# Performance work log

Measured on AMD Instinct MI355X. Metric: run time of the kernel, lower is better.

## Reference

```python
import jax, jax.numpy as jnp
import numpy as np

DIM = 192
HEADS = 8
HEAD_DIM = DIM // HEADS
SCALE = HEAD_DIM ** (-0.5)
H = W = 64
EPS = 1e-12  # F.normalize default eps


def setup_inputs() -> dict:
    key = jax.random.key(0)
    k1, k2, k3, k4 = jax.random.split(key, 4)
    x = jax.random.normal(k1, (1, DIM, H, W), jnp.float32)
    w_qkv = jax.random.normal(k2, (3 * DIM, DIM), jnp.float32) * 0.05   # 1x1 conv dim->3*dim
    w_dw = jax.random.normal(k3, (3 * DIM, 1, 3, 3), jnp.float32) * 0.05  # depthwise 3x3, groups=3*dim
    w_proj = jax.random.normal(k4, (DIM, DIM), jnp.float32) * 0.05      # 1x1 conv dim->dim
    return {"x": x, "w_qkv": w_qkv, "w_dw": w_dw, "w_proj": w_proj}


def reference(x, w_qkv, w_dw, w_proj):
    B, C, h, w = x.shape
    n = h * w
    # 1x1 conv (no bias) == channel matmul
    qkv = jnp.einsum('oc,bchw->bohw', w_qkv, x)
    # depthwise 3x3 conv, padding=1
    qkv = jax.lax.conv_general_dilated(
        qkv, w_dw, window_strides=(1, 1), padding='SAME',
        dimension_numbers=('NCHW', 'OIHW', 'NCHW'),
        feature_group_count=3 * C)
    q, k, v = jnp.split(qkv, 3, axis=1)

    def to_heads(t):  # [B,C,h,w] -> [B,heads,HW,head_dim]
        return t.reshape(B, HEADS, HEAD_DIM, n).transpose(0, 1, 3, 2)

    q, k, v = to_heads(q), to_heads(k), to_heads(v)
    # L2-normalize along head_dim (F.normalize semantics)
    q = q / jnp.maximum(jnp.linalg.norm(q, axis=-1, keepdims=True), EPS)
    k = k / jnp.maximum(jnp.linalg.norm(k, axis=-1, keepdims=True), EPS)
    attn = jax.nn.softmax(jnp.einsum('bhnd,bhmd->bhnm', q, k) * SCALE, axis=-1)
    out = jnp.einsum('bhnm,bhmd->bhnd', attn, v)  # [B,heads,HW,head_dim]
    out = out.transpose(0, 1, 3, 2).reshape(B, C, h, w)
    return jnp.einsum('oc,bchw->bohw', w_proj, out)
```

## Files before the change

kernel.cpp:

```cpp
#include <hip/hip_runtime.h>

typedef unsigned short u16;
typedef unsigned int u32;
typedef short bf16x8 __attribute__((ext_vector_type(8)));
typedef float f32x4 __attribute__((ext_vector_type(4)));
typedef float f32x16 __attribute__((ext_vector_type(16)));

__device__ __forceinline__ u16 f2bf(float f) {
  union { float f; unsigned int u; } a; a.f = f;
  unsigned int r = a.u + 0x7FFFu + ((a.u >> 16) & 1u);
  return (u16)(r >> 16);
}
__device__ __forceinline__ float bf2f(u16 b) {
  return __uint_as_float(((u32)b) << 16);
}

__global__ __launch_bounds__(256) void prep(const float* __restrict__ X,
                                            const float* __restrict__ W,
                                            const float* __restrict__ Wp,
                                            u16* __restrict__ Xt,
                                            u16* __restrict__ Wb,
                                            u16* __restrict__ Wpb) {
  int b = blockIdx.x;
  int t = threadIdx.x;
  if (b < 128) {
    __shared__ float Xl[192 * 33];
    int p0 = b << 5;
    int px = t & 31, cs = t >> 5;
    #pragma unroll
    for (int i = 0; i < 24; ++i) {
      int c = cs * 24 + i;
      Xl[c * 33 + px] = X[(size_t)c * 4096 + p0 + px];
    }
    __syncthreads();
    int pxo = t >> 3, j0 = (t & 7) * 12;
    u32* Xt32 = (u32*)Xt;
    #pragma unroll
    for (int jj = 0; jj < 12; ++jj) {
      int j = j0 + jj;
      u32 v = ((u32)f2bf(Xl[(2 * j + 1) * 33 + pxo]) << 16) |
              f2bf(Xl[(2 * j) * 33 + pxo]);
      Xt32[(size_t)(p0 + pxo) * 96 + j] = v;
    }
  } else if (b < 182) {
    int idx = (b - 128) * 2048 + t * 8;
    #pragma unroll
    for (int i = 0; i < 8; ++i) Wb[idx + i] = f2bf(W[idx + i]);
  } else {
    int idx = (b - 182) * 2048 + t * 8;
    #pragma unroll
    for (int i = 0; i < 8; ++i) Wpb[idx + i] = f2bf(Wp[idx + i]);
  }
}

template <bool B16>
__global__ __launch_bounds__(256) void mqkv(const u16* __restrict__ Wb,
                                            const u16* __restrict__ Xt,
                                            void* __restrict__ Yv) {
  __shared__ u16 Sl[4][32 * 32];
  int tid = threadIdx.x;
  int wave = tid >> 6, lane = tid & 63;
  int lo = lane & 15, hi = lane >> 4;
  int m0 = blockIdx.y << 5;
  int n0 = (blockIdx.x << 7) + (wave << 5);
  f32x4 zz = {0.f, 0.f, 0.f, 0.f};
  f32x4 acc00 = zz, acc01 = zz, acc10 = zz, acc11 = zz;
  #pragma unroll
  for (int k0 = 0; k0 < 192; k0 += 32) {
    bf16x8 a0 = *(const bf16x8*)(Wb + (size_t)(m0 + lo) * 192 + k0 + hi * 8);
    bf16x8 a1 = *(const bf16x8*)(Wb + (size_t)(m0 + 16 + lo) * 192 + k0 + hi * 8);
    bf16x8 b0 = *(const bf16x8*)(Xt + (size_t)(n0 + lo) * 192 + k0 + hi * 8);
    bf16x8 b1 = *(const bf16x8*)(Xt + (size_t)(n0 + 16 + lo) * 192 + k0 + hi * 8);
    acc00 = __builtin_amdgcn_mfma_f32_16x16x32_bf16(a0, b0, acc00, 0, 0, 0);
    acc01 = __builtin_amdgcn_mfma_f32_16x16x32_bf16(a0, b1, acc01, 0, 0, 0);
    acc10 = __builtin_amdgcn_mfma_f32_16x16x32_bf16(a1, b0, acc10, 0, 0, 0);
    acc11 = __builtin_amdgcn_mfma_f32_16x16x32_bf16(a1, b1, acc11, 0, 0, 0);
  }
  if (B16) {
    u16* S = Sl[wave];
    #pragma unroll
    for (int r = 0; r < 4; ++r) {
      S[(hi * 4 + r) * 32 + lo] = f2bf(acc00[r]);
      S[(hi * 4 + r) * 32 + 16 + lo] = f2bf(acc01[r]);
      S[(16 + hi * 4 + r) * 32 + lo] = f2bf(acc10[r]);
      S[(16 + hi * 4 + r) * 32 + 16 + lo] = f2bf(acc11[r]);
    }
    const u32* S32 = (const u32*)S;
    u32* Y32 = (u32*)Yv;
    #pragma unroll
    for (int i = lane; i < 512; i += 64) {
      int row = i >> 4, j = i & 15;
      Y32[(size_t)(m0 + row) * 2048 + (n0 >> 1) + j] = S32[row * 16 + j];
    }
  } else {
    float* Y = (float*)Yv;
    #pragma unroll
    for (int r = 0; r < 4; ++r) {
      Y[(size_t)(m0 + hi * 4 + r) * 4096 + n0 + lo] = acc00[r];
      Y[(size_t)(m0 + hi * 4 + r) * 4096 + n0 + 16 + lo] = acc01[r];
      Y[(size_t)(m0 + 16 + hi * 4 + r) * 4096 + n0 + lo] = acc10[r];
      Y[(size_t)(m0 + 16 + hi * 4 + r) * 4096 + n0 + 16 + lo] = acc11[r];
    }
  }
}

__global__ __launch_bounds__(256) void dwconv3(const u16* __restrict__ in,
                                               const float* __restrict__ w,
                                               u16* __restrict__ out) {
  int idx = blockIdx.x * 256 + threadIdx.x;
  int c = idx >> 12;
  int p = idx & 4095;
  int y = p >> 6, x = p & 63;
  const float* wc = w + c * 9;
  const u16* ic = in + (size_t)c * 4096;
  float s = 0.f;
  #pragma unroll
  for (int i = 0; i < 3; ++i) {
    int yy = y + i - 1;
    if ((unsigned)yy >= 64u) continue;
    #pragma unroll
    for (int j = 0; j < 3; ++j) {
      int xx = x + j - 1;
      if ((unsigned)xx >= 64u) continue;
      s = fmaf(wc[i * 3 + j], bf2f(ic[yy * 64 + xx]), s);
    }
  }
  out[idx] = f2bf(s);
}

__global__ __launch_bounds__(256) void nvpack(const u16* __restrict__ qkv,
                                              u32* __restrict__ Qh32,
                                              u32* __restrict__ Kh32,
                                              u32* __restrict__ Vt32) {
  __shared__ u32 Ql[128 * 17];
  __shared__ u32 Kl[128 * 17];
  __shared__ u16 Vl[32 * 128];
  int t = threadIdx.x;
  int bid = blockIdx.x;
  int h = bid >> 5;
  int p0 = (bid & 31) << 7;
  u32* Vl32 = (u32*)Vl;
  const float QSC = 0.20412414523193154f * 1.4426950408889634f;
  if (t < 128) {
    int p = p0 + t;
    float qv[24], kv[24];
    float sq = 0.f, sk = 0.f;
    #pragma unroll
    for (int d = 0; d < 24; ++d) {
      qv[d] = bf2f(qkv[(size_t)(h * 24 + d) * 4096 + p]);
      sq = fmaf(qv[d], qv[d], sq);
    }
    #pragma unroll
    for (int d = 0; d < 24; ++d) {
      kv[d] = bf2f(qkv[(size_t)(192 + h * 24 + d) * 4096 + p]);
      sk = fmaf(kv[d], kv[d], sk);
    }
    float iq = QSC / fmaxf(sqrtf(sq), 1e-12f);
    float ik = 1.0f / fmaxf(sqrtf(sk), 1e-12f);
    u32* qrow = Ql + t * 17;
    u32* krow = Kl + t * 17;
    #pragma unroll
    for (int j = 0; j < 12; ++j) {
      qrow[j] = ((u32)f2bf(qv[2 * j + 1] * iq) << 16) | f2bf(qv[2 * j] * iq);
      krow[j] = ((u32)f2bf(kv[2 * j + 1] * ik) << 16) | f2bf(kv[2 * j] * ik);
    }
    #pragma unroll
    for (int j = 12; j < 16; ++j) { qrow[j] = 0; krow[j] = 0; }
  } else {
    int tl = t - 128;
    int p = p0 + tl;
    #pragma unroll
    for (int d = 0; d < 24; ++d)
      Vl[d * 128 + tl] = qkv[(size_t)(384 + h * 24 + d) * 4096 + p];
    Vl[24 * 128 + tl] = 0x3F80;
  }
  for (int i = t; i < 7 * 64; i += 256) Vl32[25 * 64 + i] = 0;
  __syncthreads();
  size_t base = ((size_t)(h << 12) + p0) * 16;
  for (int i = t; i < 2048; i += 256) {
    u32 li = (i >> 4) * 17 + (i & 15);
    Qh32[base + i] = Ql[li];
    Kh32[base + i] = Kl[li];
  }
  for (int i = t; i < 2048; i += 256) {
    int d = i >> 6, c = i & 63;
    Vt32[(((size_t)(h * 32 + d)) << 11) + (p0 >> 1) + c] = Vl32[d * 64 + c];
  }
}

__device__ __forceinline__ void swp32(u32& a, u32& b) {
  asm("v_permlane32_swap_b32 %0, %1" : "+v"(a), "+v"(b));
}

__device__ __forceinline__ bf16x8 mkfrag(u32 a, u32 b, u32 c, u32 d) {
  union { u32 u[4]; bf16x8 v; } x;
  x.u[0] = a; x.u[1] = b; x.u[2] = c; x.u[3] = d;
  return x.v;
}

#define MFMA32(A, B, C) __builtin_amdgcn_mfma_f32_32x32x16_bf16(A, B, C, 0, 0, 0)

__global__ __launch_bounds__(512, 2) void attn(const u16* __restrict__ Qh,
                                               const u16* __restrict__ Kh,
                                               const u16* __restrict__ Vt,
                                               u16* __restrict__ Pt) {
  __shared__ float Sf[8 * 64 * 29];
  __shared__ u16 Pb[64 * 24];
  int tid = threadIdx.x;
  int wave = tid >> 6, lane = tid & 63;
  int l31 = lane & 31, h5 = lane >> 5;
  int b = blockIdx.x;
  int head = b & 7;
  int q0 = (b >> 3) << 7;

  const u16* Kb = Kh + ((size_t)head << 17);
  const u16* Vb = Vt + ((size_t)head << 17);

  size_t qbase = ((size_t)head << 12) + q0;
  bf16x8 qf[4][2];
  #pragma unroll
  for (int qb = 0; qb < 4; ++qb)
    #pragma unroll
    for (int c = 0; c < 2; ++c)
      qf[qb][c] = *(const bf16x8*)(Qh + ((qbase + qb * 32 + l31) << 5) +
                                   c * 16 + h5 * 8);

  f32x16 oC[4] = {};

  int kbase = wave << 9;

  for (int it = 0; it < 8; ++it) {
    int k0 = kbase + it * 64;
    bf16x8 kf[2][2], vf[4];
    #pragma unroll
    for (int g = 0; g < 2; ++g)
      #pragma unroll
      for (int c = 0; c < 2; ++c)
        kf[g][c] = *(const bf16x8*)(Kb + (((size_t)(k0 + g * 32 + l31)) << 5) +
                                    c * 16 + h5 * 8);
    #pragma unroll
    for (int c4 = 0; c4 < 4; ++c4)
      vf[c4] = *(const bf16x8*)(Vb + (((size_t)l31) << 12) + k0 + c4 * 16 +
                                h5 * 8);
    #pragma unroll
    for (int qb = 0; qb < 4; ++qb) {
      __builtin_amdgcn_s_setprio(1);
      f32x16 s0{}, s1{};
      s0 = MFMA32(kf[0][0], qf[qb][0], s0);
      s0 = MFMA32(kf[0][1], qf[qb][1], s0);
      s1 = MFMA32(kf[1][0], qf[qb][0], s1);
      s1 = MFMA32(kf[1][1], qf[qb][1], s1);
      __builtin_amdgcn_s_setprio(0);
      u32 w[16];
      #pragma unroll
      for (int r = 0; r < 8; ++r) {
        u32 e0 = __float_as_uint(__builtin_amdgcn_exp2f(s0[2 * r]));
        u32 e1 = __float_as_uint(__builtin_amdgcn_exp2f(s0[2 * r + 1]));
        w[r] = __builtin_amdgcn_perm(e1, e0, 0x07060302u);
        u32 e2 = __float_as_uint(__builtin_amdgcn_exp2f(s1[2 * r]));
        u32 e3 = __float_as_uint(__builtin_amdgcn_exp2f(s1[2 * r + 1]));
        w[8 + r] = __builtin_amdgcn_perm(e3, e2, 0x07060302u);
      }
      swp32(w[0], w[2]);   swp32(w[1], w[3]);
      swp32(w[4], w[6]);   swp32(w[5], w[7]);
      swp32(w[8], w[10]);  swp32(w[9], w[11]);
      swp32(w[12], w[14]); swp32(w[13], w[15]);
      __builtin_amdgcn_s_setprio(1);
      oC[qb] = MFMA32(mkfrag(w[0], w[1], w[2], w[3]), vf[0], oC[qb]);
      oC[qb] = MFMA32(mkfrag(w[4], w[5], w[6], w[7]), vf[1], oC[qb]);
      oC[qb] = MFMA32(mkfrag(w[8], w[9], w[10], w[11]), vf[2], oC[qb]);
      oC[qb] = MFMA32(mkfrag(w[12], w[13], w[14], w[15]), vf[3], oC[qb]);
      __builtin_amdgcn_s_setprio(0);
    }
  }

  const u32* Pb32 = (const u32*)Pb;
  u32* Pt32 = (u32*)Pt;
  #pragma unroll
  for (int pass = 0; pass < 2; ++pass) {
    int sb = wave * (64 * 29);
    #pragma unroll
    for (int qq = 0; qq < 2; ++qq) {
      int qb = pass * 2 + qq;
      #pragma unroll
      for (int r = 0; r < 16; ++r) {
        int row = qq * 32 + (r & 3) + 8 * (r >> 2) + 4 * h5;
        if (l31 < 25) Sf[sb + row * 29 + l31] = oC[qb][r];
      }
    }
    __syncthreads();
    int q = tid & 63;
    int d0 = tid >> 6;
    int base0 = q * 29;
    const int SS = 64 * 29;
    float den = 0.f;
    #pragma unroll
    for (int s = 0; s < 8; ++s) den += Sf[base0 + s * SS + 24];
    float inv = 1.0f / den;
    #pragma unroll
    for (int dp = 0; dp < 3; ++dp) {
      int dd = dp * 8 + d0;
      float v = 0.f;
      #pragma unroll
      for (int s = 0; s < 8; ++s) v += Sf[base0 + s * SS + dd];
      Pb[q * 24 + dd] = f2bf(v * inv);
    }
    __syncthreads();
    for (int i = tid; i < 768; i += 512) {
      int qq = i / 12, j = i - qq * 12;
      Pt32[(size_t)(q0 + pass * 64 + qq) * 96 + head * 12 + j] = Pb32[qq * 12 + j];
    }
  }
}

extern "C" void kernel_launch(void* const* d_in, const int* in_sizes, int n_in,
                              void* d_out, int out_size, void* d_ws, size_t ws_size,
                              hipStream_t stream) {
  const float* x      = (const float*)d_in[0];
  const float* w_qkv  = (const float*)d_in[1];
  const float* w_dw   = (const float*)d_in[2];
  const float* w_proj = (const float*)d_in[3];
  float* out = (float*)d_out;

  char* ws = (char*)d_ws;
  u16*   qkv    = (u16*)  (ws);
  u16*   qkvd   = (u16*)  (ws + 4718592);
  u16*   Qh     = (u16*)  (ws + 18874368);
  u16*   Kh     = (u16*)  (ws + 20971520);
  u16*   Vt     = (u16*)  (ws + 23068672);
  u16*   Xt     = (u16*)  (ws + 25165824);
  u16*   Wb     = (u16*)  (ws + 26738688);
  u16*   Wpb    = (u16*)  (ws + 26959872);
  u16*   Pt     = (u16*)  (ws + 13107200);

  prep<<<dim3(200), 256, 0, stream>>>(x, w_qkv, w_proj, Xt, Wb, Wpb);
  mqkv<true><<<dim3(32, 18), 256, 0, stream>>>(Wb, Xt, qkv);
  dwconv3<<<dim3(9216), 256, 0, stream>>>(qkv, w_dw, qkvd);
  nvpack<<<dim3(256), 256, 0, stream>>>(qkvd, (u32*)Qh, (u32*)Kh, (u32*)Vt);
  attn<<<dim3(256), 512, 0, stream>>>(Qh, Kh, Vt, Pt);
  mqkv<false><<<dim3(32, 6), 256, 0, stream>>>(Wpb, Pt, out);
}
```

Measured before the change: 121.6 us.

## Fuse depthwise 3x3 conv into the Q/K/V normalize-and-pack kernel

Merges the standalone depthwise conv kernel into the packing kernel. Each block stages a haloed tile of the 72 per-head qkv channels (four rows each) and their conv weights in shared memory, then computes the conv in registers before normalizing and packing Q, K and V. This removes one kernel launch and the write and re-read of the intermediate convolved qkv buffer. In exchange, halo rows are loaded redundantly across blocks and the larger shared-memory footprint with 384 threads may reduce occupancy.

```diff
diff --git a/kernel.cpp b/kernel.cpp
--- a/kernel.cpp
+++ b/kernel.cpp
@@ -104,34 +104,13 @@
   }
 }
 
-__global__ __launch_bounds__(256) void dwconv3(const u16* __restrict__ in,
-                                               const float* __restrict__ w,
-                                               u16* __restrict__ out) {
-  int idx = blockIdx.x * 256 + threadIdx.x;
-  int c = idx >> 12;
-  int p = idx & 4095;
-  int y = p >> 6, x = p & 63;
-  const float* wc = w + c * 9;
-  const u16* ic = in + (size_t)c * 4096;
-  float s = 0.f;
-  #pragma unroll
-  for (int i = 0; i < 3; ++i) {
-    int yy = y + i - 1;
-    if ((unsigned)yy >= 64u) continue;
-    #pragma unroll
-    for (int j = 0; j < 3; ++j) {
-      int xx = x + j - 1;
-      if ((unsigned)xx >= 64u) continue;
-      s = fmaf(wc[i * 3 + j], bf2f(ic[yy * 64 + xx]), s);
-    }
-  }
-  out[idx] = f2bf(s);
-}
-
-__global__ __launch_bounds__(256) void nvpack(const u16* __restrict__ qkv,
-                                              u32* __restrict__ Qh32,
-                                              u32* __restrict__ Kh32,
-                                              u32* __restrict__ Vt32) {
+__global__ __launch_bounds__(384) void dwnv(const u16* __restrict__ qkv,
+                                            const float* __restrict__ w_dw,
+                                            u32* __restrict__ Qh32,
+                                            u32* __restrict__ Kh32,
+                                            u32* __restrict__ Vt32) {
+  __shared__ u16 Il[72 * 4 * 64];
+  __shared__ float Wl[72 * 9];
   __shared__ u32 Ql[128 * 17];
   __shared__ u32 Kl[128 * 17];
   __shared__ u16 Vl[32 * 128];
@@ -139,50 +118,99 @@
   int bid = blockIdx.x;
   int h = bid >> 5;
   int p0 = (bid & 31) << 7;
+  int y0 = p0 >> 6;
   u32* Vl32 = (u32*)Vl;
   const float QSC = 0.20412414523193154f * 1.4426950408889634f;
+
+  const uint4* q4 = (const uint4*)qkv;
+  uint4* Il4 = (uint4*)Il;
+  for (int i = t; i < 2304; i += 384) {
+    int lc = i >> 5;
+    int rr = (i >> 3) & 3;
+    int xq = i & 7;
+    int y = y0 - 1 + rr;
+    int grp = lc / 24, rem = lc - grp * 24;
+    int g = grp * 192 + h * 24 + rem;
+    uint4 v = {0u, 0u, 0u, 0u};
+    if ((unsigned)y < 64u) v = q4[(size_t)g * 512 + y * 8 + xq];
+    Il4[lc * 32 + rr * 8 + xq] = v;
+  }
+  for (int i = t; i < 648; i += 384) {
+    int lc = i / 9, k = i - lc * 9;
+    int grp = lc / 24, rem = lc - grp * 24;
+    Wl[i] = w_dw[(grp * 192 + h * 24 + rem) * 9 + k];
+  }
+  for (int i = t; i < 448; i += 384) Vl32[25 * 64 + i] = 0;
+  __syncthreads();
+
+  int tl = t & 127;
+  int x = tl & 63, ly = tl >> 6;
+  #define CONV(lc_, out_)                                              \
+    {                                                                  \
+      const float* wc_ = Wl + (lc_) * 9;                               \
+      const u16* cb_ = Il + (lc_) * 256 + ly * 64;                     \
+      float s_ = 0.f;                                                  \
+      _Pragma("unroll")                                                \
+      for (int i_ = 0; i_ < 3; ++i_) {                                 \
+        _Pragma("unroll")                                              \
+        for (int j_ = 0; j_ < 3; ++j_) {                               \
+          int xx_ = x + j_ - 1;                                        \
+          float v_ = ((unsigned)xx_ < 64u)                             \
+                         ? bf2f(cb_[i_ * 64 + xx_]) : 0.f;             \
+          s_ = fmaf(wc_[i_ * 3 + j_], v_, s_);                         \
+        }                                                              \
+      }                                                                \
+      out_ = s_;                                                       \
+    }
   if (t < 128) {
-    int p = p0 + t;
-    float qv[24], kv[24];
-    float sq = 0.f, sk = 0.f;
+    float qv[24];
+    float sq = 0.f;
     #pragma unroll
     for (int d = 0; d < 24; ++d) {
-      qv[d] = bf2f(qkv[(size_t)(h * 24 + d) * 4096 + p]);
+      CONV(d, qv[d]);
       sq = fmaf(qv[d], qv[d], sq);
     }
+    float iq = QSC / fmaxf(sqrtf(sq), 1e-12f);
+    u32* qrow = Ql + tl * 17;
+    #pragma unroll
+    for (int j = 0; j < 12; ++j)
+      qrow[j] = ((u32)f2bf(qv[2 * j + 1] * iq) << 16) | f2bf(qv[2 * j] * iq);
+    #pragma unroll
+    for (int j = 12; j < 16; ++j) qrow[j] = 0;
+  } else if (t < 256) {
+    float kv[24];
+    float sk = 0.f;
     #pragma unroll
     for (int d = 0; d < 24; ++d) {
-      kv[d] = bf2f(qkv[(size_t)(192 + h * 24 + d) * 4096 + p]);
+      CONV(24 + d, kv[d]);
       sk = fmaf(kv[d], kv[d], sk);
     }
-    float iq = QSC / fmaxf(sqrtf(sq), 1e-12f);
     float ik = 1.0f / fmaxf(sqrtf(sk), 1e-12f);
-    u32* qrow = Ql + t * 17;
-    u32* krow = Kl + t * 17;
-    #pragma unroll
-    for (int j = 0; j < 12; ++j) {
-      qrow[j] = ((u32)f2bf(qv[2 * j + 1] * iq) << 16) | f2bf(qv[2 * j] * iq);
+    u32* krow = Kl + tl * 17;
+    #pragma unroll
+    for (int j = 0; j < 12; ++j)
       krow[j] = ((u32)f2bf(kv[2 * j + 1] * ik) << 16) | f2bf(kv[2 * j] * ik);
-    }
-    #pragma unroll
-    for (int j = 12; j < 16; ++j) { qrow[j] = 0; krow[j] = 0; }
+    #pragma unroll
+    for (int j = 12; j < 16; ++j) krow[j] = 0;
   } else {
-    int tl = t - 128;
-    int p = p0 + tl;
-    #pragma unroll
-    for (int d = 0; d < 24; ++d)
-      Vl[d * 128 + tl] = qkv[(size_t)(384 + h * 24 + d) * 4096 + p];
+    #pragma unroll
+    for (int d = 0; d < 24; ++d) {
+      float vv;
+      CONV(48 + d, vv);
+      Vl[d * 128 + tl] = f2bf(vv);
+    }
     Vl[24 * 128 + tl] = 0x3F80;
   }
-  for (int i = t; i < 7 * 64; i += 256) Vl32[25 * 64 + i] = 0;
+  #undef CONV
   __syncthreads();
+
   size_t base = ((size_t)(h << 12) + p0) * 16;
-  for (int i = t; i < 2048; i += 256) {
+  for (int i = t; i < 2048; i += 384) {
     u32 li = (i >> 4) * 17 + (i & 15);
     Qh32[base + i] = Ql[li];
     Kh32[base + i] = Kl[li];
   }
-  for (int i = t; i < 2048; i += 256) {
+  for (int i = t; i < 2048; i += 384) {
     int d = i >> 6, c = i & 63;
     Vt32[(((size_t)(h * 32 + d)) << 11) + (p0 >> 1) + c] = Vl32[d * 64 + c];
   }
@@ -324,7 +352,6 @@
 
   char* ws = (char*)d_ws;
   u16*   qkv    = (u16*)  (ws);
-  u16*   qkvd   = (u16*)  (ws + 4718592);
   u16*   Qh     = (u16*)  (ws + 18874368);
   u16*   Kh     = (u16*)  (ws + 20971520);
   u16*   Vt     = (u16*)  (ws + 23068672);
@@ -335,8 +362,7 @@
 
   prep<<<dim3(200), 256, 0, stream>>>(x, w_qkv, w_proj, Xt, Wb, Wpb);
   mqkv<true><<<dim3(32, 18), 256, 0, stream>>>(Wb, Xt, qkv);
-  dwconv3<<<dim3(9216), 256, 0, stream>>>(qkv, w_dw, qkvd);
-  nvpack<<<dim3(256), 256, 0, stream>>>(qkvd, (u32*)Qh, (u32*)Kh, (u32*)Vt);
+  dwnv<<<dim3(256), 384, 0, stream>>>(qkv, w_dw, (u32*)Qh, (u32*)Kh, (u32*)Vt);
   attn<<<dim3(256), 512, 0, stream>>>(Qh, Kh, Vt, Pt);
   mqkv<false><<<dim3(32, 6), 256, 0, stream>>>(Wpb, Pt, out);
 }
```

Measured after the change: 152.2 us. +25.1%, slower.
